# Optimization experiments

Measured on AMD Instinct MI355X. Metric: run time of the kernel, lower is better.

Reference implementation:

```python
import jax, jax.numpy as jnp
import numpy as np

NX, NY = 8192, 8192
C1, C2, D = 2048, 2048, 512

def setup_inputs() -> dict:
    key = jax.random.key(0)
    k1, k2, k3, k4, k5 = jax.random.split(key, 5)
    scale1 = 1.0 / np.sqrt(C1)
    scale2 = 1.0 / np.sqrt(C2)
    return {
        "x": jax.random.normal(k1, (NX, C1), dtype=jnp.float32),
        "y": jax.random.normal(k2, (NY, C2), dtype=jnp.float32),
        "Wq": jax.random.uniform(k3, (D, C1), dtype=jnp.float32, minval=-scale1, maxval=scale1),
        "Wk": jax.random.uniform(k4, (D, C2), dtype=jnp.float32, minval=-scale2, maxval=scale2),
        "Wv": jax.random.uniform(k5, (D, C2), dtype=jnp.float32, minval=-scale2, maxval=scale2),
    }

def reference(x, y, Wq, Wk, Wv):
    d = Wq.shape[0]
    q = x @ Wq.T                      # [nx, d]
    k = y @ Wk.T                      # [ny, d]
    v = y @ Wv.T                      # [ny, d]
    a = (q @ k.T) * (d ** -0.5)       # [nx, ny]
    # torch.triu(ones) masks upper triangle INCLUDING diagonal -> zero where j >= i
    nx, ny = a.shape
    i = jnp.arange(nx)[:, None]
    j = jnp.arange(ny)[None, :]
    a = jnp.where(j >= i, 0.0, a)
    return a @ v                      # [nx, d]
```

## Files before the change

### kernel.cpp

```cpp
#include <hip/hip_runtime.h>
#include <hip/hip_bf16.h>


typedef __bf16 bf16x8 __attribute__((ext_vector_type(8)));
typedef __bf16 bf16x4 __attribute__((ext_vector_type(4)));
typedef __bf16 bf16x2 __attribute__((ext_vector_type(2)));
typedef float f32x4 __attribute__((ext_vector_type(4)));

#define MFMA16(a, b, c) __builtin_amdgcn_mfma_f32_16x16x32_bf16(a, b, c, 0, 0, 0)

constexpr float SCALE = 0.04419417382415922f;

__device__ __forceinline__ void ld16(const void* g, void* l) {
    __builtin_amdgcn_global_load_lds(
        (__attribute__((address_space(1))) void*)g,
        (__attribute__((address_space(3))) void*)l, 16, 0, 0);
}

__device__ __forceinline__ bf16x8 frag(const __bf16* base, int r, int c) {
    return *(const bf16x8*)((const char*)base + r * 128 + ((c ^ (r & 7)) * 16));
}

__device__ __forceinline__ bf16x8 fragA32(const float* base, int r, int c0) {
    const char* rowp = (const char*)base + r * 256;
    f32x4 a = *(const f32x4*)(rowp + ((c0 ^ (r & 15)) * 16));
    f32x4 b = *(const f32x4*)(rowp + (((c0 + 1) ^ (r & 15)) * 16));
    bf16x8 o;
    o[0] = (__bf16)a[0]; o[1] = (__bf16)a[1];
    o[2] = (__bf16)a[2]; o[3] = (__bf16)a[3];
    o[4] = (__bf16)b[0]; o[5] = (__bf16)b[1];
    o[6] = (__bf16)b[2]; o[7] = (__bf16)b[3];
    return o;
}

__device__ inline bf16x4 pack4(float4 a) {
    bf16x4 r;
    r[0] = (__bf16)a.x; r[1] = (__bf16)a.y;
    r[2] = (__bf16)a.z; r[3] = (__bf16)a.w;
    return r;
}

__global__ __launch_bounds__(256) void convert_w(
    const float* __restrict__ wqf, const float* __restrict__ wkf,
    const float* __restrict__ wvf, __bf16* __restrict__ wqb,
    __bf16* __restrict__ wkb, __bf16* __restrict__ wvb)
{
    const size_t tid = (size_t)blockIdx.x * 256 + threadIdx.x;
    const size_t w = tid >> 6;
    const int lane = (int)(tid & 63);
    size_t f = w * 512;
    const float* src; __bf16* dst;
    if (f < 1048576)      { src = wqf; dst = wqb; }
    else if (f < 2097152) { src = wkf; dst = wkb; f -= 1048576; }
    else                  { src = wvf; dst = wvb; f -= 2097152; }
    const float4* s4 = (const float4*)(src + f);
    float4 a = s4[lane];
    float4 b = s4[64 + lane];
    __bf16* d = dst + f;
    *(bf16x4*)(d + lane * 4)       = pack4(a);
    *(bf16x4*)(d + 256 + lane * 4) = pack4(b);
}

__global__ __launch_bounds__(256, 2) void gemm_qkv2(
    const float* __restrict__ x, const float* __restrict__ y,
    const __bf16* __restrict__ wq, const __bf16* __restrict__ wk,
    const __bf16* __restrict__ wv, __bf16* __restrict__ qo,
    __bf16* __restrict__ ko, __bf16* __restrict__ kT,
    __bf16* __restrict__ vT)
{
    constexpr int K = 2048, N = 512;
    __shared__ __align__(16) float  Asf[128][64];
    __shared__ __align__(16) __bf16 Bs[2][128][64];

    const bool iskv = (blockIdx.y & 1) != 0;
    const float* A = iskv ? y : x;
    const __bf16* B0 = iskv ? wk : wq;

    const int tid  = threadIdx.x;
    const int wave = tid >> 6, lane = tid & 63;
    const int fr = lane & 15, fq = lane >> 4;
    const int m0 = blockIdx.x * 128, n0 = (blockIdx.y >> 1) * 128;
    const int wr = (wave >> 1) * 64, wc = (wave & 1) * 64;
    const int lr = lane >> 3;
    const int cd = (lane & 7) ^ lr;
    const int lr4 = lane >> 4;
    const int cl  = lane & 15;

    f32x4 acc0[4][4], acc1[4][4];
#pragma unroll
    for (int a = 0; a < 4; ++a)
#pragma unroll
        for (int b = 0; b < 4; ++b) {
            acc0[a][b] = f32x4{0.f, 0.f, 0.f, 0.f};
            acc1[a][b] = f32x4{0.f, 0.f, 0.f, 0.f};
        }

    const __bf16* bg0 = B0 + (size_t)(n0 + wave * 32 + lr) * K + cd * 8;
    const __bf16* bg1 = wv + (size_t)(n0 + wave * 32 + lr) * K + cd * 8;
    float*  alf = &Asf[wave * 32][0];
    __bf16* bl0 = &Bs[0][wave * 32][0];
    __bf16* bl1 = &Bs[1][wave * 32][0];
    const float* ag0 = A + (size_t)(m0 + wave * 32 + lr4) * K;

    for (int kk = 0; kk < K; kk += 64) {
        __syncthreads();
#pragma unroll
        for (int u = 0; u < 4; ++u)
            ld16(bg0 + (size_t)(u * 8) * K + kk, bl0 + u * 512);
        if (iskv) {
#pragma unroll
            for (int u = 0; u < 4; ++u)
                ld16(bg1 + (size_t)(u * 8) * K + kk, bl1 + u * 512);
        }
#pragma unroll
        for (int u = 0; u < 8; ++u) {
            const int rw = u * 4 + lr4;
            const int c  = cl ^ (rw & 15);
            ld16(ag0 + (size_t)(u * 4) * K + kk + c * 4, alf + u * 256);
        }
        __syncthreads();
#pragma unroll
        for (int ks = 0; ks < 2; ++ks) {
            bf16x8 af[4], bf[4];
#pragma unroll
            for (int rt = 0; rt < 4; ++rt)
                af[rt] = fragA32(&Asf[0][0], wr + rt * 16 + fr, ks * 8 + fq * 2);
#pragma unroll
            for (int nt = 0; nt < 4; ++nt)
                bf[nt] = frag(&Bs[0][0][0], wc + nt * 16 + fr, ks * 4 + fq);
#pragma unroll
            for (int rt = 0; rt < 4; ++rt)
#pragma unroll
                for (int nt = 0; nt < 4; ++nt)
                    acc0[rt][nt] = MFMA16(af[rt], bf[nt], acc0[rt][nt]);
            if (iskv) {
                bf16x8 bg[4];
#pragma unroll
                for (int nt = 0; nt < 4; ++nt)
                    bg[nt] = frag(&Bs[1][0][0], wc + nt * 16 + fr, ks * 4 + fq);
#pragma unroll
                for (int rt = 0; rt < 4; ++rt)
#pragma unroll
                    for (int nt = 0; nt < 4; ++nt)
                        acc1[rt][nt] = MFMA16(af[rt], bg[nt], acc1[rt][nt]);
            }
        }
    }

    if (!iskv) {
#pragma unroll
        for (int rt = 0; rt < 4; ++rt)
#pragma unroll
            for (int nt = 0; nt < 4; ++nt) {
                const int col = n0 + wc + nt * 16 + fr;
#pragma unroll
                for (int r = 0; r < 4; ++r) {
                    const int row = m0 + wr + rt * 16 + fq * 4 + r;
                    qo[(size_t)row * N + col] = (__bf16)(acc0[rt][nt][r] * SCALE);
                }
            }
    } else {
#pragma unroll
        for (int rt = 0; rt < 4; ++rt)
#pragma unroll
            for (int nt = 0; nt < 4; ++nt) {
                const int col  = n0 + wc + nt * 16 + fr;
                const int row0 = m0 + wr + rt * 16 + fq * 4;
                bf16x4 k4, v4;
#pragma unroll
                for (int r = 0; r < 4; ++r) {
                    k4[r] = (__bf16)acc0[rt][nt][r];
                    v4[r] = (__bf16)acc1[rt][nt][r];
                    ko[(size_t)(row0 + r) * N + col] = k4[r];
                }
                *(bf16x4*)(kT + (size_t)col * 8192 + row0) = k4;
                *(bf16x4*)(vT + (size_t)col * 8192 + row0) = v4;
            }
    }
}

__global__ __launch_bounds__(256, 3) void hs_gemm(
    const __bf16* __restrict__ vT, const __bf16* __restrict__ kT,
    const __bf16* __restrict__ q, const __bf16* __restrict__ k,
    __bf16* __restrict__ Ht, __bf16* __restrict__ Sd)
{
    __shared__ __align__(16) __bf16 As[128][64];
    __shared__ __align__(16) __bf16 Bs[128][64];

    const int tid  = threadIdx.x;
    const int wave = tid >> 6, lane = tid & 63;
    const int fr = lane & 15, fq = lane >> 4;
    const int wr = (wave >> 1) * 64, wc = (wave & 1) * 64;
    const int lr = lane >> 3;
    const int cd = (lane & 7) ^ lr;

    f32x4 acc[4][4];
#pragma unroll
    for (int a = 0; a < 4; ++a)
#pragma unroll
        for (int b = 0; b < 4; ++b) acc[a][b] = f32x4{0.f, 0.f, 0.f, 0.f};

    __bf16* al = &As[wave * 32][0];
    __bf16* bl = &Bs[wave * 32][0];

    if (blockIdx.y < 63) {
        const int c  = blockIdx.y;
        const int m0 = (blockIdx.x & 3) * 128;
        const int n0 = (blockIdx.x >> 2) * 128;

        const __bf16* ag = vT + (size_t)(m0 + wave * 32 + lr) * 8192 + c * 128 + cd * 8;
        const __bf16* bg = kT + (size_t)(n0 + wave * 32 + lr) * 8192 + c * 128 + cd * 8;

        for (int kk = 0; kk < 128; kk += 64) {
            __syncthreads();
#pragma unroll
            for (int u = 0; u < 4; ++u) {
                ld16(ag + (size_t)(u * 8) * 8192 + kk, al + u * 512);
                ld16(bg + (size_t)(u * 8) * 8192 + kk, bl + u * 512);
            }
            __syncthreads();
#pragma unroll
            for (int ks = 0; ks < 2; ++ks) {
                bf16x8 af[4], bf[4];
#pragma unroll
                for (int rt = 0; rt < 4; ++rt)
                    af[rt] = frag(&As[0][0], wr + rt * 16 + fr, ks * 4 + fq);
#pragma unroll
                for (int nt = 0; nt < 4; ++nt)
                    bf[nt] = frag(&Bs[0][0], wc + nt * 16 + fr, ks * 4 + fq);
#pragma unroll
                for (int rt = 0; rt < 4; ++rt)
#pragma unroll
                    for (int nt = 0; nt < 4; ++nt)
                        acc[rt][nt] = MFMA16(af[rt], bf[nt], acc[rt][nt]);
            }
        }

        __bf16* tp = Ht + (size_t)c * 262144;
#pragma unroll
        for (int rt = 0; rt < 4; ++rt)
#pragma unroll
            for (int nt = 0; nt < 4; ++nt) {
                const int col = n0 + wc + nt * 16 + fr;
#pragma unroll
                for (int r = 0; r < 4; ++r) {
                    const int row = m0 + wr + rt * 16 + fq * 4 + r;
                    tp[(size_t)row * 512 + col] = (__bf16)acc[rt][nt][r];
                }
            }
    } else {
        const int t = (blockIdx.y - 63) * 16 + blockIdx.x;

        const __bf16* ag = q + (size_t)(t * 128 + wave * 32 + lr) * 512 + cd * 8;
        const __bf16* bg = k + (size_t)(t * 128 + wave * 32 + lr) * 512 + cd * 8;

        for (int kk = 0; kk < 512; kk += 64) {
            __syncthreads();
#pragma unroll
            for (int u = 0; u < 4; ++u) {
                ld16(ag + (size_t)(u * 8) * 512 + kk, al + u * 512);
                ld16(bg + (size_t)(u * 8) * 512 + kk, bl + u * 512);
            }
            __syncthreads();
#pragma unroll
            for (int ks = 0; ks < 2; ++ks) {
                bf16x8 af[4], bf[4];
#pragma unroll
                for (int rt = 0; rt < 4; ++rt)
                    af[rt] = frag(&As[0][0], wr + rt * 16 + fr, ks * 4 + fq);
#pragma unroll
                for (int nt = 0; nt < 4; ++nt)
                    bf[nt] = frag(&Bs[0][0], wc + nt * 16 + fr, ks * 4 + fq);
#pragma unroll
                for (int rt = 0; rt < 4; ++rt)
#pragma unroll
                    for (int nt = 0; nt < 4; ++nt)
                        acc[rt][nt] = MFMA16(af[rt], bf[nt], acc[rt][nt]);
            }
        }

        __bf16* tp = Sd + (size_t)t * 16384;
#pragma unroll
        for (int rt = 0; rt < 4; ++rt)
#pragma unroll
            for (int nt = 0; nt < 4; ++nt) {
                const int col = wc + nt * 16 + fr;
#pragma unroll
                for (int r = 0; r < 4; ++r) {
                    const int row = wr + rt * 16 + fq * 4 + r;
                    float vv = (col < row) ? acc[rt][nt][r] : 0.f;
                    tp[row * 128 + col] = (__bf16)vv;
                }
            }
    }
}

__global__ __launch_bounds__(256) void prefix_scan(
    const __bf16* __restrict__ Ht, __bf16* __restrict__ Pt)
{
    const size_t e = ((size_t)blockIdx.x * 256 + threadIdx.x) * 2;
    float a0 = 0.f, a1 = 0.f;
#pragma unroll 9
    for (int c = 0; c < 63; ++c) {
        bf16x2 h = *(const bf16x2*)(Ht + (size_t)c * 262144 + e);
        a0 += (float)h[0]; a1 += (float)h[1];
        bf16x2 p;
        p[0] = (__bf16)a0; p[1] = (__bf16)a1;
        *(bf16x2*)(Pt + (size_t)(c + 1) * 262144 + e) = p;
    }
}

__global__ __launch_bounds__(256, 3) void out_gemm(
    const __bf16* __restrict__ q, const __bf16* __restrict__ Sd,
    const __bf16* __restrict__ vT, const __bf16* __restrict__ Pt,
    float* __restrict__ out)
{
    __shared__ __align__(16) __bf16 As[128][64];
    __shared__ __align__(16) __bf16 Bs[128][64];

    const int t  = blockIdx.x;
    const int n0 = blockIdx.y * 128;

    const int tid  = threadIdx.x;
    const int wave = tid >> 6, lane = tid & 63;
    const int fr = lane & 15, fq = lane >> 4;
    const int wr = (wave >> 1) * 64, wc = (wave & 1) * 64;
    const int lr = lane >> 3;
    const int cd = (lane & 7) ^ lr;
    const int srow = wave * 32 + lr;

    f32x4 acc[4][4];
#pragma unroll
    for (int a = 0; a < 4; ++a)
#pragma unroll
        for (int b = 0; b < 4; ++b) acc[a][b] = f32x4{0.f, 0.f, 0.f, 0.f};

    __bf16* al = &As[wave * 32][0];
    __bf16* bl = &Bs[wave * 32][0];

    if (t > 0) {
        const __bf16* ag = q + (size_t)(t * 128 + srow) * 512 + cd * 8;
        const __bf16* bg2 = Pt + (size_t)t * 262144
                          + (size_t)(n0 + srow) * 512 + cd * 8;
        for (int kk = 0; kk < 512; kk += 64) {
            __syncthreads();
#pragma unroll
            for (int u = 0; u < 4; ++u) {
                ld16(ag + (size_t)(u * 8) * 512 + kk, al + u * 512);
                ld16(bg2 + (size_t)(u * 8) * 512 + kk, bl + u * 512);
            }
            __syncthreads();
#pragma unroll
            for (int ks = 0; ks < 2; ++ks) {
                bf16x8 af[4], bf[4];
#pragma unroll
                for (int rt = 0; rt < 4; ++rt)
                    af[rt] = frag(&As[0][0], wr + rt * 16 + fr, ks * 4 + fq);
#pragma unroll
                for (int nt = 0; nt < 4; ++nt)
                    bf[nt] = frag(&Bs[0][0], wc + nt * 16 + fr, ks * 4 + fq);
#pragma unroll
                for (int rt = 0; rt < 4; ++rt)
#pragma unroll
                    for (int nt = 0; nt < 4; ++nt)
                        acc[rt][nt] = MFMA16(af[rt], bf[nt], acc[rt][nt]);
            }
        }
    }

    const __bf16* at3 = Sd + (size_t)t * 16384 + (size_t)srow * 128 + cd * 8;
    const __bf16* bg3 = vT + (size_t)(n0 + srow) * 8192 + t * 128 + cd * 8;
    for (int kk = 0; kk < 128; kk += 64) {
        __syncthreads();
#pragma unroll
        for (int u = 0; u < 4; ++u) {
            ld16(at3 + (size_t)(u * 8) * 128 + kk, al + u * 512);
            ld16(bg3 + (size_t)(u * 8) * 8192 + kk, bl + u * 512);
        }
        __syncthreads();
#pragma unroll
        for (int ks = 0; ks < 2; ++ks) {
            bf16x8 af[4], bf[4];
#pragma unroll
            for (int rt = 0; rt < 4; ++rt)
                af[rt] = frag(&As[0][0], wr + rt * 16 + fr, ks * 4 + fq);
#pragma unroll
            for (int nt = 0; nt < 4; ++nt)
                bf[nt] = frag(&Bs[0][0], wc + nt * 16 + fr, ks * 4 + fq);
#pragma unroll
            for (int rt = 0; rt < 4; ++rt)
#pragma unroll
                for (int nt = 0; nt < 4; ++nt)
                    acc[rt][nt] = MFMA16(af[rt], bf[nt], acc[rt][nt]);
        }
    }

#pragma unroll
    for (int rt = 0; rt < 4; ++rt)
#pragma unroll
        for (int nt = 0; nt < 4; ++nt) {
            const int col = n0 + wc + nt * 16 + fr;
#pragma unroll
            for (int r = 0; r < 4; ++r) {
                const int row = t * 128 + wr + rt * 16 + fq * 4 + r;
                out[(size_t)row * 512 + col] = acc[rt][nt][r];
            }
        }
}

extern "C" void kernel_launch(void* const* d_in, const int* in_sizes, int n_in,
                              void* d_out, int out_size, void* d_ws, size_t ws_size,
                              hipStream_t stream) {
    const float* x  = (const float*)d_in[0];
    const float* y  = (const float*)d_in[1];
    const float* Wq = (const float*)d_in[2];
    const float* Wk = (const float*)d_in[3];
    const float* Wv = (const float*)d_in[4];
    float* out = (float*)d_out;

    const size_t QK = (size_t)8192 * 512;
    __bf16* q  = (__bf16*)d_ws;
    __bf16* k  = q + QK;
    __bf16* kT = k + QK;
    __bf16* vT = kT + QK;
    __bf16* Ht  = vT + QK;
    __bf16* Pt  = Ht + 16777216;
    __bf16* wqb = Pt + 16777216;
    __bf16* wkb = wqb + 1048576;
    __bf16* wvb = wkb + 1048576;
    __bf16* Sd = wqb;

    convert_w<<<1536, 256, 0, stream>>>(Wq, Wk, Wv, wqb, wkb, wvb);
    gemm_qkv2<<<dim3(64, 8), 256, 0, stream>>>(x, y, wqb, wkb, wvb, q, k, kT, vT);
    hs_gemm<<<dim3(16, 67), 256, 0, stream>>>(vT, kT, q, k, Ht, Sd);
    prefix_scan<<<512, 256, 0, stream>>>(Ht, Pt);
    out_gemm<<<dim3(64, 4), 256, 0, stream>>>(q, Sd, vT, Pt, out);
}
```

Before: 253.5 us.

## Fuse Q, K and V projections into one block with three accumulators

The QKV projection kernel now has each block compute Q from x and both K and V from y for the same 128x128 tile, using 112 KB of dynamic shared memory and three accumulator sets. The grid drops from 512 to 256 blocks, and a new XCD-aware tile mapping assigns contiguous row tiles per XCD to improve L2 reuse. Previously half the blocks did only one GEMM while the other half did two, so work was imbalanced. The cost is occupancy: one block per CU with high register pressure, and only 256 blocks to spread across the CUs.

```diff
diff --git a/kernel.cpp b/kernel.cpp
--- a/kernel.cpp
+++ b/kernel.cpp
@@ -61,7 +61,7 @@
     *(bf16x4*)(d + 256 + lane * 4) = pack4(b);
 }
 
-__global__ __launch_bounds__(256, 2) void gemm_qkv2(
+__global__ __launch_bounds__(256, 1) void gemm_qkv3(
     const float* __restrict__ x, const float* __restrict__ y,
     const __bf16* __restrict__ wq, const __bf16* __restrict__ wk,
     const __bf16* __restrict__ wv, __bf16* __restrict__ qo,
@@ -69,114 +69,106 @@
     __bf16* __restrict__ vT)
 {
     constexpr int K = 2048, N = 512;
-    __shared__ __align__(16) float  Asf[128][64];
-    __shared__ __align__(16) __bf16 Bs[2][128][64];
-
-    const bool iskv = (blockIdx.y & 1) != 0;
-    const float* A = iskv ? y : x;
-    const __bf16* B0 = iskv ? wk : wq;
+    extern __shared__ char smem[];
+    float*  Ax = (float*)smem;
+    float*  Ay = (float*)(smem + 32768);
+    __bf16* Bq = (__bf16*)(smem + 65536);
+    __bf16* Bk = (__bf16*)(smem + 81920);
+    __bf16* Bv = (__bf16*)(smem + 98304);
+
+    const int lin = blockIdx.y * 64 + blockIdx.x;
+    const int xcd = lin & 7, idx = lin >> 3;
+    const int m0 = (xcd * 8 + (idx & 7)) * 128;
+    const int n0 = (idx >> 3) * 128;
 
     const int tid  = threadIdx.x;
     const int wave = tid >> 6, lane = tid & 63;
     const int fr = lane & 15, fq = lane >> 4;
-    const int m0 = blockIdx.x * 128, n0 = (blockIdx.y >> 1) * 128;
     const int wr = (wave >> 1) * 64, wc = (wave & 1) * 64;
     const int lr = lane >> 3;
     const int cd = (lane & 7) ^ lr;
     const int lr4 = lane >> 4;
     const int cl  = lane & 15;
 
-    f32x4 acc0[4][4], acc1[4][4];
+    f32x4 aq[4][4], ak[4][4], av[4][4];
 #pragma unroll
     for (int a = 0; a < 4; ++a)
 #pragma unroll
         for (int b = 0; b < 4; ++b) {
-            acc0[a][b] = f32x4{0.f, 0.f, 0.f, 0.f};
-            acc1[a][b] = f32x4{0.f, 0.f, 0.f, 0.f};
-        }
-
-    const __bf16* bg0 = B0 + (size_t)(n0 + wave * 32 + lr) * K + cd * 8;
-    const __bf16* bg1 = wv + (size_t)(n0 + wave * 32 + lr) * K + cd * 8;
-    float*  alf = &Asf[wave * 32][0];
-    __bf16* bl0 = &Bs[0][wave * 32][0];
-    __bf16* bl1 = &Bs[1][wave * 32][0];
-    const float* ag0 = A + (size_t)(m0 + wave * 32 + lr4) * K;
+            aq[a][b] = f32x4{0.f, 0.f, 0.f, 0.f};
+            ak[a][b] = f32x4{0.f, 0.f, 0.f, 0.f};
+            av[a][b] = f32x4{0.f, 0.f, 0.f, 0.f};
+        }
+
+    const float*  agx = x  + (size_t)(m0 + wave * 32 + lr4) * K;
+    const float*  agy = y  + (size_t)(m0 + wave * 32 + lr4) * K;
+    const __bf16* bgq = wq + (size_t)(n0 + wave * 32 + lr) * K + cd * 8;
+    const __bf16* bgk = wk + (size_t)(n0 + wave * 32 + lr) * K + cd * 8;
+    const __bf16* bgv = wv + (size_t)(n0 + wave * 32 + lr) * K + cd * 8;
+    float*  axl = Ax + wave * 2048;
+    float*  ayl = Ay + wave * 2048;
+    __bf16* bql = Bq + wave * 2048;
+    __bf16* bkl = Bk + wave * 2048;
+    __bf16* bvl = Bv + wave * 2048;
 
     for (int kk = 0; kk < K; kk += 64) {
         __syncthreads();
 #pragma unroll
-        for (int u = 0; u < 4; ++u)
-            ld16(bg0 + (size_t)(u * 8) * K + kk, bl0 + u * 512);
-        if (iskv) {
-#pragma unroll
-            for (int u = 0; u < 4; ++u)
-                ld16(bg1 + (size_t)(u * 8) * K + kk, bl1 + u * 512);
+        for (int u = 0; u < 4; ++u) {
+            ld16(bgq + (size_t)(u * 8) * K + kk, bql + u * 512);
+            ld16(bgk + (size_t)(u * 8) * K + kk, bkl + u * 512);
+            ld16(bgv + (size_t)(u * 8) * K + kk, bvl + u * 512);
         }
 #pragma unroll
         for (int u = 0; u < 8; ++u) {
             const int rw = u * 4 + lr4;
             const int c  = cl ^ (rw & 15);
-            ld16(ag0 + (size_t)(u * 4) * K + kk + c * 4, alf + u * 256);
+            ld16(agx + (size_t)(u * 4) * K + kk + c * 4, axl + u * 256);
+            ld16(agy + (size_t)(u * 4) * K + kk + c * 4, ayl + u * 256);
         }
         __syncthreads();
 #pragma unroll
         for (int ks = 0; ks < 2; ++ks) {
-            bf16x8 af[4], bf[4];
+            bf16x8 fx[4], fy[4], bq_[4], bk_[4], bv_[4];
+#pragma unroll
+            for (int rt = 0; rt < 4; ++rt) {
+                fx[rt] = fragA32(Ax, wr + rt * 16 + fr, ks * 8 + fq * 2);
+                fy[rt] = fragA32(Ay, wr + rt * 16 + fr, ks * 8 + fq * 2);
+            }
+#pragma unroll
+            for (int nt = 0; nt < 4; ++nt) {
+                bq_[nt] = frag(Bq, wc + nt * 16 + fr, ks * 4 + fq);
+                bk_[nt] = frag(Bk, wc + nt * 16 + fr, ks * 4 + fq);
+                bv_[nt] = frag(Bv, wc + nt * 16 + fr, ks * 4 + fq);
+            }
 #pragma unroll
             for (int rt = 0; rt < 4; ++rt)
-                af[rt] = fragA32(&Asf[0][0], wr + rt * 16 + fr, ks * 8 + fq * 2);
-#pragma unroll
-            for (int nt = 0; nt < 4; ++nt)
-                bf[nt] = frag(&Bs[0][0][0], wc + nt * 16 + fr, ks * 4 + fq);
-#pragma unroll
-            for (int rt = 0; rt < 4; ++rt)
-#pragma unroll
-                for (int nt = 0; nt < 4; ++nt)
-                    acc0[rt][nt] = MFMA16(af[rt], bf[nt], acc0[rt][nt]);
-            if (iskv) {
-                bf16x8 bg[4];
-#pragma unroll
-                for (int nt = 0; nt < 4; ++nt)
-                    bg[nt] = frag(&Bs[1][0][0], wc + nt * 16 + fr, ks * 4 + fq);
-#pragma unroll
-                for (int rt = 0; rt < 4; ++rt)
-#pragma unroll
-                    for (int nt = 0; nt < 4; ++nt)
-                        acc1[rt][nt] = MFMA16(af[rt], bg[nt], acc1[rt][nt]);
-            }
-        }
-    }
-
-    if (!iskv) {
-#pragma unroll
-        for (int rt = 0; rt < 4; ++rt)
-#pragma unroll
-            for (int nt = 0; nt < 4; ++nt) {
-                const int col = n0 + wc + nt * 16 + fr;
-#pragma unroll
-                for (int r = 0; r < 4; ++r) {
-                    const int row = m0 + wr + rt * 16 + fq * 4 + r;
-                    qo[(size_t)row * N + col] = (__bf16)(acc0[rt][nt][r] * SCALE);
+#pragma unroll
+                for (int nt = 0; nt < 4; ++nt) {
+                    aq[rt][nt] = MFMA16(fx[rt], bq_[nt], aq[rt][nt]);
+                    ak[rt][nt] = MFMA16(fy[rt], bk_[nt], ak[rt][nt]);
+                    av[rt][nt] = MFMA16(fy[rt], bv_[nt], av[rt][nt]);
                 }
-            }
-    } else {
-#pragma unroll
-        for (int rt = 0; rt < 4; ++rt)
-#pragma unroll
-            for (int nt = 0; nt < 4; ++nt) {
-                const int col  = n0 + wc + nt * 16 + fr;
-                const int row0 = m0 + wr + rt * 16 + fq * 4;
-                bf16x4 k4, v4;
-#pragma unroll
-                for (int r = 0; r < 4; ++r) {
-                    k4[r] = (__bf16)acc0[rt][nt][r];
-                    v4[r] = (__bf16)acc1[rt][nt][r];
-                    ko[(size_t)(row0 + r) * N + col] = k4[r];
-                }
-                *(bf16x4*)(kT + (size_t)col * 8192 + row0) = k4;
-                *(bf16x4*)(vT + (size_t)col * 8192 + row0) = v4;
-            }
-    }
+        }
+    }
+
+#pragma unroll
+    for (int rt = 0; rt < 4; ++rt)
+#pragma unroll
+        for (int nt = 0; nt < 4; ++nt) {
+            const int col  = n0 + wc + nt * 16 + fr;
+            const int row0 = m0 + wr + rt * 16 + fq * 4;
+            bf16x4 k4, v4;
+#pragma unroll
+            for (int r = 0; r < 4; ++r) {
+                qo[(size_t)(row0 + r) * N + col] = (__bf16)(aq[rt][nt][r] * SCALE);
+                k4[r] = (__bf16)ak[rt][nt][r];
+                v4[r] = (__bf16)av[rt][nt][r];
+                ko[(size_t)(row0 + r) * N + col] = k4[r];
+            }
+            *(bf16x4*)(kT + (size_t)col * 8192 + row0) = k4;
+            *(bf16x4*)(vT + (size_t)col * 8192 + row0) = v4;
+        }
 }
 
 __global__ __launch_bounds__(256, 3) void hs_gemm(
@@ -430,8 +422,16 @@
     __bf16* wvb = wkb + 1048576;
     __bf16* Sd = wqb;
 
+    const int smem = 114688;
+    static bool attr_done = false;
+    if (!attr_done) {
+        hipFuncSetAttribute((const void*)gemm_qkv3,
+                            hipFuncAttributeMaxDynamicSharedMemorySize, smem);
+        attr_done = true;
+    }
+
     convert_w<<<1536, 256, 0, stream>>>(Wq, Wk, Wv, wqb, wkb, wvb);
-    gemm_qkv2<<<dim3(64, 8), 256, 0, stream>>>(x, y, wqb, wkb, wvb, q, k, kT, vT);
+    gemm_qkv3<<<dim3(64, 4), 256, smem, stream>>>(x, y, wqb, wkb, wvb, q, k, kT, vT);
     hs_gemm<<<dim3(16, 67), 256, 0, stream>>>(vT, kT, q, k, Ht, Sd);
     prefix_scan<<<512, 256, 0, stream>>>(Ht, Pt);
     out_gemm<<<dim3(64, 4), 256, 0, stream>>>(q, Sd, vT, Pt, out);
```

New measurement: 297.0 us. 17.2% more time.
